# Optimization experiments

Measured on AMD Instinct MI355X. Metric: run time of the kernel, lower is better.

Reference implementation:

```python
import jax, jax.numpy as jnp
import numpy as np

N = 50000          # nodes
E = 800000         # edges (avg degree 16)
IN, HID, OUT = 128, 128, 64
LAMBDA_MAX = 2.0   # DGL default convention for scaled Laplacian (re_norm = 2/lambda_max = 1)


def setup_inputs() -> dict:
    key = jax.random.key(0)
    k1, k2, k3, k4, k5 = jax.random.split(key, 5)
    features = jax.random.normal(k1, (N, IN), dtype=jnp.float32)
    src = jax.random.randint(k2, (E,), 0, N)
    dst = jax.random.randint(k3, (E,), 0, N)
    # ChebConv(k=2) linear: Linear(2*in, out), torch default uniform init
    s1 = 1.0 / np.sqrt(2 * IN)
    W1 = jax.random.uniform(k4, (2 * IN, HID), jnp.float32, -s1, s1)
    b1 = jnp.zeros((HID,), jnp.float32)
    s2 = 1.0 / np.sqrt(2 * HID)
    W2 = jax.random.uniform(k5, (2 * HID, OUT), jnp.float32, -s2, s2)
    b2 = jnp.zeros((OUT,), jnp.float32)
    return {"features": features, "src": src, "dst": dst,
            "W1": W1, "b1": b1, "W2": W2, "b2": b2}


def _cheb_conv(x, src, dst, d_invsqrt, W, b, re_norm):
    msg = (x * d_invsqrt)[src]                                   # [E, d]
    h = jax.ops.segment_sum(msg, dst, num_segments=N) * d_invsqrt  # [N, d]
    # X_1 = L_tilde X_0 = -re_norm * A_hat X + (re_norm - 1) * X
    x1 = -re_norm * h + x * (re_norm - 1.0)
    xt = jnp.concatenate([x, x1], axis=1)                        # [N, 2d]
    return xt @ W + b


def reference(features, src, dst, W1, b1, W2, b2):
    deg = jax.ops.segment_sum(jnp.ones((E,), jnp.float32), dst, num_segments=N)
    d_invsqrt = jnp.power(jnp.clip(deg, 1.0, None), -0.5)[:, None]  # [N,1]
    re_norm = 2.0 / LAMBDA_MAX
    h = _cheb_conv(features, src, dst, d_invsqrt, W1, b1, re_norm)
    # dropout omitted (eval mode)
    h = _cheb_conv(h, src, dst, d_invsqrt, W2, b2, re_norm)
    return h
```

## Files before the change

kernel.cpp:

```cpp
#include <hip/hip_runtime.h>

#define IN_DIM  128

typedef __bf16 bf16x8 __attribute__((ext_vector_type(8)));
typedef float  f32x4  __attribute__((ext_vector_type(4)));

static inline size_t align256(size_t x) { return (x + 255) & ~size_t(255); }

__device__ __forceinline__ ushort f2b1(float f) {
    union { float f; uint u; } c; c.f = f;
    uint u = c.u;
    uint r = (u + 0x7FFFu + ((u >> 16) & 1u)) >> 16;
    return (ushort)r;
}
__device__ __forceinline__ float lo_bf(uint v) {
    union { uint u; float f; } c; c.u = v << 16; return c.f;
}
__device__ __forceinline__ float hi_bf(uint v) {
    union { uint u; float f; } c; c.u = v & 0xffff0000u; return c.f;
}


__global__ void zero_kernel(int4* __restrict__ p, int n16) {
    int i = blockIdx.x * blockDim.x + threadIdx.x;
    if (i < n16) p[i] = make_int4(0, 0, 0, 0);
}

__global__ void hist_kernel(const int* __restrict__ dst, int* __restrict__ deg,
                            int* __restrict__ rank, int E) {
    int e = blockIdx.x * blockDim.x + threadIdx.x;
    if (e < E) rank[e] = atomicAdd(&deg[dst[e]], 1);
}

__global__ __launch_bounds__(256) void scan_blocks(const int* __restrict__ deg,
                                                   int* __restrict__ pre,
                                                   int* __restrict__ bsum, int n) {
    __shared__ int sh[256];
    int t = threadIdx.x;
    int base = blockIdx.x * 1024 + t * 4;
    int v0 = 0, v1 = 0, v2 = 0, v3 = 0;
    if (base + 3 < n) {
        int4 v = *reinterpret_cast<const int4*>(deg + base);
        v0 = v.x; v1 = v.y; v2 = v.z; v3 = v.w;
    } else {
        if (base     < n) v0 = deg[base];
        if (base + 1 < n) v1 = deg[base + 1];
        if (base + 2 < n) v2 = deg[base + 2];
        if (base + 3 < n) v3 = deg[base + 3];
    }
    int s = v0 + v1 + v2 + v3;
    sh[t] = s;
    __syncthreads();
    for (int off = 1; off < 256; off <<= 1) {
        int x = (t >= off) ? sh[t - off] : 0;
        __syncthreads();
        sh[t] += x;
        __syncthreads();
    }
    int excl = sh[t] - s;
    if (t == 255) bsum[blockIdx.x] = sh[255];
    if (base     < n) pre[base]     = excl;
    if (base + 1 < n) pre[base + 1] = excl + v0;
    if (base + 2 < n) pre[base + 2] = excl + v0 + v1;
    if (base + 3 < n) pre[base + 3] = excl + v0 + v1 + v2;
}

__global__ __launch_bounds__(256) void scan_add(
    const int* __restrict__ pre, const int* __restrict__ bsum,
    const int* __restrict__ deg,
    int* __restrict__ rowptr, float* __restrict__ dinv,
    int n, int E, int nb)
{
    __shared__ int sb[64];
    int t = threadIdx.x;
    if (t < 64) {
        int orig = (t < nb) ? bsum[t] : 0;
        int v = orig;
        for (int off = 1; off < 64; off <<= 1) {
            int u = __shfl_up(v, off);
            if (t >= off) v += u;
        }
        sb[t] = v - orig;
    }
    __syncthreads();
    int i = blockIdx.x * blockDim.x + t;
    if (i < n) {
        rowptr[i] = pre[i] + sb[i >> 10];
        int d = deg[i]; if (d < 1) d = 1;
        dinv[i] = rsqrtf((float)d);
    }
    if (i == 0) rowptr[n] = E;
}


template <typename CT>
__global__ __launch_bounds__(256) void phase2_kernel(
    const int* __restrict__ src, const int* __restrict__ dst,
    const int* __restrict__ rowptr, const int* __restrict__ rank,
    CT* __restrict__ col, int E, int fillBlocks,
    const float* __restrict__ feats, const float* __restrict__ dinv,
    ushort* __restrict__ featb, ushort* __restrict__ featbs,
    ushort* __restrict__ z2s, int N, int nbF,
    const float* __restrict__ W1, ushort* __restrict__ W1t,
    const float* __restrict__ W2, ushort* __restrict__ W2ct)
{
    int b = blockIdx.x, t = threadIdx.x;
    if (b < fillBlocks) {
        int e0 = (b * 256 + t) * 4;
        if (e0 + 3 < E) {
            int4 d4 = *reinterpret_cast<const int4*>(dst + e0);
            int4 r4 = *reinterpret_cast<const int4*>(rank + e0);
            int4 s4 = *reinterpret_cast<const int4*>(src + e0);
            col[rowptr[d4.x] + r4.x] = (CT)s4.x;
            col[rowptr[d4.y] + r4.y] = (CT)s4.y;
            col[rowptr[d4.z] + r4.z] = (CT)s4.z;
            col[rowptr[d4.w] + r4.w] = (CT)s4.w;
        } else {
            for (int e = e0; e < E; ++e)
                col[rowptr[dst[e]] + rank[e]] = (CT)src[e];
        }
        return;
    }
    int b2 = b - fillBlocks;
    if (b2 < nbF) {
        size_t i4 = (size_t)b2 * 256 + t;
        if (i4 < (size_t)N * 32) {
            size_t i = i4 * 4;
            float4 v = *reinterpret_cast<const float4*>(feats + i);
            float dv = dinv[i >> 7];
            ushort4 o, os;
            o.x  = f2b1(v.x);      o.y  = f2b1(v.y);      o.z  = f2b1(v.z);      o.w  = f2b1(v.w);
            os.x = f2b1(v.x * dv); os.y = f2b1(v.y * dv); os.z = f2b1(v.z * dv); os.w = f2b1(v.w * dv);
            *reinterpret_cast<ushort4*>(featb  + i) = o;
            *reinterpret_cast<ushort4*>(featbs + i) = os;
        }
    } else if (b2 < nbF + 128) {
        if (b2 == nbF) {
            if (t < 32) *reinterpret_cast<uint2*>(featbs + (size_t)N * 128 + t * 4) = make_uint2(0, 0);
            else if (t < 48) *reinterpret_cast<uint2*>(z2s + (size_t)N * 64 + (t - 32) * 4) = make_uint2(0, 0);
        }
        int i = (b2 - nbF) * 256 + t;
        int k = i >> 7, c = i & 127;
        W1t[(size_t)c * 256 + k] = f2b1(W1[i]);
    } else {
        int i = (b2 - nbF - 128) * 256 + t;
        int c = i >> 7, k = i & 127;
        float v = (c < 64) ? W2[(size_t)k * 64 + c]
                           : W2[(size_t)(128 + k) * 64 + (c - 64)];
        W2ct[(size_t)c * 128 + k] = f2b1(v);
    }
}


__device__ __forceinline__ void sum16(
    const uint* __restrict__ Xu, int lane, int slane, int coff,
    float& a0, float& a1)
{
    uint v[16];
    #pragma unroll
    for (int j = 0; j < 16; ++j) {
        int s = __builtin_amdgcn_readlane(slane, coff + j);
        v[j] = Xu[(uint)(s * 64 + lane)];
    }
    #pragma unroll
    for (int j = 0; j < 16; ++j) {
        a0 += lo_bf(v[j]);
        a1 += hi_bf(v[j]);
    }
}

template <typename CT>
__global__ __launch_bounds__(256) void agg_sum128(
    const ushort* __restrict__ Xs, const int* __restrict__ rowptr,
    const CT* __restrict__ col, const float* __restrict__ dinv,
    ushort* __restrict__ X1, int nNodes)
{
    int wid  = (blockIdx.x * blockDim.x + threadIdx.x) >> 6;
    int lane = threadIdx.x & 63;
    if (wid >= nNodes) return;
    wid = __builtin_amdgcn_readfirstlane(wid);
    int e0 = rowptr[wid], e1 = rowptr[wid + 1];
    float sc = -dinv[wid];
    const uint* Xu = reinterpret_cast<const uint*>(Xs);

    float a0 = 0.f, a1 = 0.f;
    for (int base = e0; base < e1; base += 64) {
        int idx = base + lane;
        int s = (idx < e1) ? (int)col[(idx < e1) ? idx : e0] : nNodes;
        int cnt = e1 - base; if (cnt > 64) cnt = 64;
        sum16(Xu, lane, s, 0, a0, a1);
        if (cnt > 16) sum16(Xu, lane, s, 16, a0, a1);
        if (cnt > 32) sum16(Xu, lane, s, 32, a0, a1);
        if (cnt > 48) sum16(Xu, lane, s, 48, a0, a1);
    }
    uint o = (uint)f2b1(a0 * sc) | ((uint)f2b1(a1 * sc) << 16);
    reinterpret_cast<uint*>(X1)[(uint)(wid * 64 + lane)] = o;
}


__device__ __forceinline__ void sum16z(
    const ushort* __restrict__ Z, int lane, int slane, int coff, float& a0)
{
    ushort v[16];
    #pragma unroll
    for (int j = 0; j < 16; ++j) {
        int s = __builtin_amdgcn_readlane(slane, coff + j);
        v[j] = Z[(uint)(s * 64 + lane)];
    }
    #pragma unroll
    for (int j = 0; j < 16; ++j)
        a0 += lo_bf((uint)v[j]);
}

template <typename CT>
__global__ __launch_bounds__(256) void agg_sum64(
    const ushort* __restrict__ Z2, const int* __restrict__ rowptr,
    const CT* __restrict__ col, const float* __restrict__ dinv,
    float* __restrict__ Y, int nNodes)
{
    int wid  = (blockIdx.x * blockDim.x + threadIdx.x) >> 6;
    int lane = threadIdx.x & 63;
    if (wid >= nNodes) return;
    wid = __builtin_amdgcn_readfirstlane(wid);
    int e0 = rowptr[wid], e1 = rowptr[wid + 1];
    float sc = -dinv[wid];

    float a0 = 0.f;
    for (int base = e0; base < e1; base += 64) {
        int idx = base + lane;
        int s = (idx < e1) ? (int)col[(idx < e1) ? idx : e0] : nNodes;
        int cnt = e1 - base; if (cnt > 64) cnt = 64;
        sum16z(Z2, lane, s, 0, a0);
        if (cnt > 16) sum16z(Z2, lane, s, 16, a0);
        if (cnt > 32) sum16z(Z2, lane, s, 32, a0);
        if (cnt > 48) sum16z(Z2, lane, s, 48, a0);
    }
    Y[(uint)(wid * 64 + lane)] += a0 * sc;
}


__global__ __launch_bounds__(256) void gemm_mfma1(
    const ushort* __restrict__ XA, const ushort* __restrict__ XB,
    const ushort* __restrict__ Wt, const float* __restrict__ bias,
    ushort* __restrict__ Y, int nNodes)
{
    __shared__ ushort wlds[128 * 256];
    int t = threadIdx.x;

    #pragma unroll
    for (int it = 0; it < 16; ++it) {
        int i = it * 256 + t;
        int c = i >> 5;
        int o = (i & 31) << 4;
        bf16x8 v = *reinterpret_cast<const bf16x8*>(Wt + ((size_t)c << 8) + (o >> 1));
        *reinterpret_cast<bf16x8*>((char*)wlds + ((size_t)c << 9) + (o ^ ((c & 7) << 4))) = v;
    }
    __syncthreads();

    int wave = t >> 6, lane = t & 63;
    int r16 = lane & 15, g = lane >> 4;
    int nodeBase = blockIdx.x * 128 + wave * 32;

    int arow0 = nodeBase + r16;       if (arow0 > nNodes - 1) arow0 = nNodes - 1;
    int arow1 = nodeBase + 16 + r16;  if (arow1 > nNodes - 1) arow1 = nNodes - 1;
    const ushort* pA0 = XA + (size_t)arow0 * 128;
    const ushort* pA1 = XA + (size_t)arow1 * 128;
    const ushort* pB0 = XB + (size_t)arow0 * 128;
    const ushort* pB1 = XB + (size_t)arow1 * 128;

    f32x4 acc0[8], acc1[8];
    #pragma unroll
    for (int i = 0; i < 8; ++i) { acc0[i] = f32x4{0,0,0,0}; acc1[i] = f32x4{0,0,0,0}; }

    #pragma unroll
    for (int kb = 0; kb < 8; ++kb) {
        int kk = (kb & 3) * 32 + g * 8;
        bf16x8 a0 = *reinterpret_cast<const bf16x8*>(((kb < 4) ? pA0 : pB0) + kk);
        bf16x8 a1 = *reinterpret_cast<const bf16x8*>(((kb < 4) ? pA1 : pB1) + kk);
        int o = kb * 64 + g * 16;
        #pragma unroll
        for (int ct = 0; ct < 8; ++ct) {
            int c = ct * 16 + r16;
            bf16x8 b = *reinterpret_cast<const bf16x8*>(
                (const char*)wlds + ((size_t)c << 9) + (o ^ ((c & 7) << 4)));
            acc0[ct] = __builtin_amdgcn_mfma_f32_16x16x32_bf16(a0, b, acc0[ct], 0, 0, 0);
            acc1[ct] = __builtin_amdgcn_mfma_f32_16x16x32_bf16(a1, b, acc1[ct], 0, 0, 0);
        }
    }

    #pragma unroll
    for (int ct = 0; ct < 8; ++ct) {
        float bv = bias[ct * 16 + r16];
        #pragma unroll
        for (int r = 0; r < 4; ++r) {
            int orow0 = nodeBase + g * 4 + r;
            int orow1 = orow0 + 16;
            if (orow0 < nNodes) Y[(size_t)orow0 * 128 + ct * 16 + r16] = f2b1(acc0[ct][r] + bv);
            if (orow1 < nNodes) Y[(size_t)orow1 * 128 + ct * 16 + r16] = f2b1(acc1[ct][r] + bv);
        }
    }
}


__global__ __launch_bounds__(256) void gemm_mfma2(
    const ushort* __restrict__ H1, const ushort* __restrict__ W2ct,
    const float* __restrict__ bias, const float* __restrict__ dinv,
    float* __restrict__ Yout, ushort* __restrict__ Z2, int nNodes)
{
    __shared__ ushort wlds[128 * 128];
    int t = threadIdx.x;

    #pragma unroll
    for (int it = 0; it < 8; ++it) {
        int i = it * 256 + t;
        int c = i >> 4;
        int o = (i & 15) << 4;
        bf16x8 v = *reinterpret_cast<const bf16x8*>(W2ct + ((size_t)c << 7) + (o >> 1));
        *reinterpret_cast<bf16x8*>((char*)wlds + ((size_t)c << 8) + (o ^ ((c & 7) << 4))) = v;
    }
    __syncthreads();

    int wave = t >> 6, lane = t & 63;
    int r16 = lane & 15, g = lane >> 4;
    int nodeBase = blockIdx.x * 128 + wave * 32;

    int arow0 = nodeBase + r16;       if (arow0 > nNodes - 1) arow0 = nNodes - 1;
    int arow1 = nodeBase + 16 + r16;  if (arow1 > nNodes - 1) arow1 = nNodes - 1;
    const ushort* p0 = H1 + (size_t)arow0 * 128;
    const ushort* p1 = H1 + (size_t)arow1 * 128;

    f32x4 acc0[8], acc1[8];
    #pragma unroll
    for (int i = 0; i < 8; ++i) { acc0[i] = f32x4{0,0,0,0}; acc1[i] = f32x4{0,0,0,0}; }

    #pragma unroll
    for (int kb = 0; kb < 4; ++kb) {
        int kk = kb * 32 + g * 8;
        bf16x8 a0 = *reinterpret_cast<const bf16x8*>(p0 + kk);
        bf16x8 a1 = *reinterpret_cast<const bf16x8*>(p1 + kk);
        int o = kb * 64 + g * 16;
        #pragma unroll
        for (int ct = 0; ct < 8; ++ct) {
            int c = ct * 16 + r16;
            bf16x8 b = *reinterpret_cast<const bf16x8*>(
                (const char*)wlds + ((size_t)c << 8) + (o ^ ((c & 7) << 4)));
            acc0[ct] = __builtin_amdgcn_mfma_f32_16x16x32_bf16(a0, b, acc0[ct], 0, 0, 0);
            acc1[ct] = __builtin_amdgcn_mfma_f32_16x16x32_bf16(a1, b, acc1[ct], 0, 0, 0);
        }
    }

    float dv0[4], dv1[4];
    #pragma unroll
    for (int r = 0; r < 4; ++r) {
        int o0 = nodeBase + g * 4 + r;      if (o0 > nNodes - 1) o0 = nNodes - 1;
        int o1 = nodeBase + 16 + g * 4 + r; if (o1 > nNodes - 1) o1 = nNodes - 1;
        dv0[r] = dinv[o0]; dv1[r] = dinv[o1];
    }

    #pragma unroll
    for (int ct = 0; ct < 8; ++ct) {
        float bv = (ct < 4) ? bias[ct * 16 + r16] : 0.f;
        #pragma unroll
        for (int r = 0; r < 4; ++r) {
            int orow0 = nodeBase + g * 4 + r;
            int orow1 = orow0 + 16;
            if (ct < 4) {
                if (orow0 < nNodes) Yout[(size_t)orow0 * 64 + ct * 16 + r16] = acc0[ct][r] + bv;
                if (orow1 < nNodes) Yout[(size_t)orow1 * 64 + ct * 16 + r16] = acc1[ct][r] + bv;
            } else {
                if (orow0 < nNodes) Z2[(size_t)orow0 * 64 + (ct - 4) * 16 + r16] = f2b1(acc0[ct][r] * dv0[r]);
                if (orow1 < nNodes) Z2[(size_t)orow1 * 64 + (ct - 4) * 16 + r16] = f2b1(acc1[ct][r] * dv1[r]);
            }
        }
    }
}


extern "C" void kernel_launch(void* const* d_in, const int* in_sizes, int n_in,
                              void* d_out, int out_size, void* d_ws, size_t ws_size,
                              hipStream_t stream)
{
    const float* feats = (const float*)d_in[0];
    const int*   src   = (const int*)d_in[1];
    const int*   dst   = (const int*)d_in[2];
    const float* W1    = (const float*)d_in[3];
    const float* b1    = (const float*)d_in[4];
    const float* W2    = (const float*)d_in[5];
    const float* b2    = (const float*)d_in[6];
    float* out = (float*)d_out;

    const int N = in_sizes[0] / IN_DIM;
    const int E = in_sizes[1];
    const int NB = (N + 1023) / 1024;

    char* ws = (char*)d_ws;
    size_t off = 0;
    int*    deg    = (int*)(ws + off);    off = align256(off + (size_t)N * 4);
    int*    rowptr = (int*)(ws + off);    off = align256(off + (size_t)(N + 1) * 4);
    int*    pre    = (int*)(ws + off);    off = align256(off + (size_t)N * 4);
    int*    bsum   = (int*)(ws + off);    off = align256(off + (size_t)64 * 4);
    int*    rank   = (int*)(ws + off);    off = align256(off + (size_t)E * 4);
    void*   colv   = (void*)(ws + off);   off = align256(off + (size_t)E * 4);
    float*  dinv   = (float*)(ws + off);  off = align256(off + (size_t)N * 4);
    ushort* featb  = (ushort*)(ws + off); off = align256(off + (size_t)N * 128 * 2);
    ushort* featbs = (ushort*)(ws + off); off = align256(off + (size_t)(N + 1) * 128 * 2);
    ushort* x1b    = (ushort*)(ws + off); off = align256(off + (size_t)N * 128 * 2);
    ushort* h1b    = (ushort*)(ws + off); off = align256(off + (size_t)N * 128 * 2);
    ushort* z2s    = (ushort*)(ws + off); off = align256(off + (size_t)(N + 1) * 64 * 2);
    ushort* W1t    = (ushort*)(ws + off); off = align256(off + (size_t)256 * 128 * 2);
    ushort* W2ct   = (ushort*)(ws + off); off = align256(off + (size_t)128 * 128 * 2);

    const int n16 = (N + 3) / 4;
    zero_kernel<<<(n16 + 255) / 256, 256, 0, stream>>>((int4*)deg, n16);
    hist_kernel<<<(E + 255) / 256, 256, 0, stream>>>(dst, deg, rank, E);
    scan_blocks<<<NB, 256, 0, stream>>>(deg, pre, bsum, N);
    scan_add<<<(N + 255) / 256, 256, 0, stream>>>(pre, bsum, deg, rowptr, dinv, N, E, NB);

    const bool small = (N <= 65535);
    const int fillBlocks = ((E + 3) / 4 + 255) / 256;
    const int nbF = (N * 32 + 255) / 256;
    const int p2Blocks = fillBlocks + nbF + 128 + 64;
    if (small)
        phase2_kernel<ushort><<<p2Blocks, 256, 0, stream>>>(
            src, dst, rowptr, rank, (ushort*)colv, E, fillBlocks,
            feats, dinv, featb, featbs, z2s, N, nbF, W1, W1t, W2, W2ct);
    else
        phase2_kernel<uint><<<p2Blocks, 256, 0, stream>>>(
            src, dst, rowptr, rank, (uint*)colv, E, fillBlocks,
            feats, dinv, featb, featbs, z2s, N, nbF, W1, W1t, W2, W2ct);

    const int aggBlocks = (N * 64 + 255) / 256;
    const int gemmBlocks = (N + 127) / 128;

    if (small)
        agg_sum128<ushort><<<aggBlocks, 256, 0, stream>>>(featbs, rowptr, (const ushort*)colv, dinv, x1b, N);
    else
        agg_sum128<uint><<<aggBlocks, 256, 0, stream>>>(featbs, rowptr, (const uint*)colv, dinv, x1b, N);
    gemm_mfma1<<<gemmBlocks, 256, 0, stream>>>(featb, x1b, W1t, b1, h1b, N);

    gemm_mfma2<<<gemmBlocks, 256, 0, stream>>>(h1b, W2ct, b2, dinv, out, z2s, N);
    if (small)
        agg_sum64<ushort><<<aggBlocks, 256, 0, stream>>>(z2s, rowptr, (const ushort*)colv, dinv, out, N);
    else
        agg_sum64<uint><<<aggBlocks, 256, 0, stream>>>(z2s, rowptr, (const uint*)colv, dinv, out, N);
}
```

Baseline: 145.9 us.

## Split gathered feature tables into 64-byte column blocks for cache-local aggregation

```diff
diff --git a/kernel.cpp b/kernel.cpp
--- a/kernel.cpp
+++ b/kernel.cpp
@@ -99,8 +99,8 @@
     const int* __restrict__ rowptr, const int* __restrict__ rank,
     CT* __restrict__ col, int E, int fillBlocks,
     const float* __restrict__ feats, const float* __restrict__ dinv,
-    ushort* __restrict__ featb, ushort* __restrict__ featbs,
-    ushort* __restrict__ z2s, int N, int nbF,
+    ushort* __restrict__ featb, ushort* __restrict__ featbs2,
+    ushort* __restrict__ z2s2, int N, int nbF,
     const float* __restrict__ W1, ushort* __restrict__ W1t,
     const float* __restrict__ W2, ushort* __restrict__ W2ct)
 {
@@ -127,17 +127,26 @@
         if (i4 < (size_t)N * 32) {
             size_t i = i4 * 4;
             float4 v = *reinterpret_cast<const float4*>(feats + i);
-            float dv = dinv[i >> 7];
+            int node = (int)(i4 >> 5);
+            int j = (int)(i4 & 31);
+            float dv = dinv[node];
             ushort4 o, os;
             o.x  = f2b1(v.x);      o.y  = f2b1(v.y);      o.z  = f2b1(v.z);      o.w  = f2b1(v.w);
             os.x = f2b1(v.x * dv); os.y = f2b1(v.y * dv); os.z = f2b1(v.z * dv); os.w = f2b1(v.w * dv);
-            *reinterpret_cast<ushort4*>(featb  + i) = o;
-            *reinterpret_cast<ushort4*>(featbs + i) = os;
+            *reinterpret_cast<ushort4*>(featb + i) = o;
+            int blk = j >> 3, jj = j & 7;
+            *reinterpret_cast<ushort4*>(featbs2 + ((size_t)(blk * (N + 1) + node)) * 32 + jj * 4) = os;
         }
     } else if (b2 < nbF + 128) {
-        if (b2 == nbF) {
-            if (t < 32) *reinterpret_cast<uint2*>(featbs + (size_t)N * 128 + t * 4) = make_uint2(0, 0);
-            else if (t < 48) *reinterpret_cast<uint2*>(z2s + (size_t)N * 64 + (t - 32) * 4) = make_uint2(0, 0);
+        if (b2 == nbF && t < 48) {
+            if (t < 32) {
+                int blk = t >> 3, j = t & 7;
+                *reinterpret_cast<uint2*>(featbs2 + ((size_t)(blk * (N + 1) + N)) * 32 + j * 4) = make_uint2(0, 0);
+            } else {
+                int tt = t - 32;
+                int blk = tt >> 3, j = tt & 7;
+                *reinterpret_cast<uint2*>(z2s2 + ((size_t)(blk * (N + 1) + N)) * 32 + j * 4) = make_uint2(0, 0);
+            }
         }
         int i = (b2 - nbF) * 256 + t;
         int k = i >> 7, c = i & 127;
@@ -152,25 +161,25 @@
 }
 
 
-__device__ __forceinline__ void sum16(
-    const uint* __restrict__ Xu, int lane, int slane, int coff,
+__device__ __forceinline__ void grp4(
+    const uint* __restrict__ base, int sl, int g, int d, int eslot,
     float& a0, float& a1)
 {
-    uint v[16];
-    #pragma unroll
-    for (int j = 0; j < 16; ++j) {
-        int s = __builtin_amdgcn_readlane(slane, coff + j);
-        v[j] = Xu[(uint)(s * 64 + lane)];
-    }
-    #pragma unroll
-    for (int j = 0; j < 16; ++j) {
-        a0 += lo_bf(v[j]);
-        a1 += hi_bf(v[j]);
+    uint v[4];
+    #pragma unroll
+    for (int c = 0; c < 4; ++c) {
+        int s = __shfl(sl, g * 16 + c * 4 + eslot);
+        v[c] = base[(uint)(s * 16 + d)];
+    }
+    #pragma unroll
+    for (int c = 0; c < 4; ++c) {
+        a0 += lo_bf(v[c]);
+        a1 += hi_bf(v[c]);
     }
 }
 
 template <typename CT>
-__global__ __launch_bounds__(256) void agg_sum128(
+__global__ __launch_bounds__(256) void agg1_blk(
     const ushort* __restrict__ Xs, const int* __restrict__ rowptr,
     const CT* __restrict__ col, const float* __restrict__ dinv,
     ushort* __restrict__ X1, int nNodes)
@@ -178,64 +187,69 @@
     int wid  = (blockIdx.x * blockDim.x + threadIdx.x) >> 6;
     int lane = threadIdx.x & 63;
     if (wid >= nNodes) return;
-    wid = __builtin_amdgcn_readfirstlane(wid);
-    int e0 = rowptr[wid], e1 = rowptr[wid + 1];
-    float sc = -dinv[wid];
-    const uint* Xu = reinterpret_cast<const uint*>(Xs);
+    int n = __builtin_amdgcn_readfirstlane(wid);
+    int b = blockIdx.y;
+    int e0 = rowptr[n], e1 = rowptr[n + 1];
+    float sc = -dinv[n];
+    const uint* base = reinterpret_cast<const uint*>(Xs) + (size_t)b * (nNodes + 1) * 16;
+    int d = lane & 15, eslot = lane >> 4;
 
     float a0 = 0.f, a1 = 0.f;
-    for (int base = e0; base < e1; base += 64) {
-        int idx = base + lane;
-        int s = (idx < e1) ? (int)col[(idx < e1) ? idx : e0] : nNodes;
-        int cnt = e1 - base; if (cnt > 64) cnt = 64;
-        sum16(Xu, lane, s, 0, a0, a1);
-        if (cnt > 16) sum16(Xu, lane, s, 16, a0, a1);
-        if (cnt > 32) sum16(Xu, lane, s, 32, a0, a1);
-        if (cnt > 48) sum16(Xu, lane, s, 48, a0, a1);
-    }
-    uint o = (uint)f2b1(a0 * sc) | ((uint)f2b1(a1 * sc) << 16);
-    reinterpret_cast<uint*>(X1)[(uint)(wid * 64 + lane)] = o;
-}
-
-
-__device__ __forceinline__ void sum16z(
-    const ushort* __restrict__ Z, int lane, int slane, int coff, float& a0)
-{
-    ushort v[16];
-    #pragma unroll
-    for (int j = 0; j < 16; ++j) {
-        int s = __builtin_amdgcn_readlane(slane, coff + j);
-        v[j] = Z[(uint)(s * 64 + lane)];
-    }
-    #pragma unroll
-    for (int j = 0; j < 16; ++j)
-        a0 += lo_bf((uint)v[j]);
+    for (int bs = e0; bs < e1; bs += 64) {
+        int idx = bs + lane;
+        int ci = (idx < e1) ? idx : e0;
+        int cv = (int)col[ci];
+        int sl = (idx < e1) ? cv : nNodes;
+        int cnt = e1 - bs; if (cnt > 64) cnt = 64;
+        grp4(base, sl, 0, d, eslot, a0, a1);
+        if (cnt > 16) grp4(base, sl, 1, d, eslot, a0, a1);
+        if (cnt > 32) grp4(base, sl, 2, d, eslot, a0, a1);
+        if (cnt > 48) grp4(base, sl, 3, d, eslot, a0, a1);
+    }
+    a0 += __shfl_xor(a0, 16); a0 += __shfl_xor(a0, 32);
+    a1 += __shfl_xor(a1, 16); a1 += __shfl_xor(a1, 32);
+    if (eslot == 0) {
+        uint o = (uint)f2b1(a0 * sc) | ((uint)f2b1(a1 * sc) << 16);
+        reinterpret_cast<uint*>(X1)[(uint)(n * 64 + b * 16 + d)] = o;
+    }
 }
 
 template <typename CT>
-__global__ __launch_bounds__(256) void agg_sum64(
-    const ushort* __restrict__ Z2, const int* __restrict__ rowptr,
+__global__ __launch_bounds__(256) void agg2_blk(
+    const ushort* __restrict__ Zs, const int* __restrict__ rowptr,
     const CT* __restrict__ col, const float* __restrict__ dinv,
     float* __restrict__ Y, int nNodes)
 {
     int wid  = (blockIdx.x * blockDim.x + threadIdx.x) >> 6;
     int lane = threadIdx.x & 63;
     if (wid >= nNodes) return;
-    wid = __builtin_amdgcn_readfirstlane(wid);
-    int e0 = rowptr[wid], e1 = rowptr[wid + 1];
-    float sc = -dinv[wid];
-
-    float a0 = 0.f;
-    for (int base = e0; base < e1; base += 64) {
-        int idx = base + lane;
-        int s = (idx < e1) ? (int)col[(idx < e1) ? idx : e0] : nNodes;
-        int cnt = e1 - base; if (cnt > 64) cnt = 64;
-        sum16z(Z2, lane, s, 0, a0);
-        if (cnt > 16) sum16z(Z2, lane, s, 16, a0);
-        if (cnt > 32) sum16z(Z2, lane, s, 32, a0);
-        if (cnt > 48) sum16z(Z2, lane, s, 48, a0);
-    }
-    Y[(uint)(wid * 64 + lane)] += a0 * sc;
+    int n = __builtin_amdgcn_readfirstlane(wid);
+    int b = blockIdx.y;
+    int e0 = rowptr[n], e1 = rowptr[n + 1];
+    float sc = -dinv[n];
+    const uint* base = reinterpret_cast<const uint*>(Zs) + (size_t)b * (nNodes + 1) * 16;
+    int d = lane & 15, eslot = lane >> 4;
+
+    float a0 = 0.f, a1 = 0.f;
+    for (int bs = e0; bs < e1; bs += 64) {
+        int idx = bs + lane;
+        int ci = (idx < e1) ? idx : e0;
+        int cv = (int)col[ci];
+        int sl = (idx < e1) ? cv : nNodes;
+        int cnt = e1 - bs; if (cnt > 64) cnt = 64;
+        grp4(base, sl, 0, d, eslot, a0, a1);
+        if (cnt > 16) grp4(base, sl, 1, d, eslot, a0, a1);
+        if (cnt > 32) grp4(base, sl, 2, d, eslot, a0, a1);
+        if (cnt > 48) grp4(base, sl, 3, d, eslot, a0, a1);
+    }
+    a0 += __shfl_xor(a0, 16); a0 += __shfl_xor(a0, 32);
+    a1 += __shfl_xor(a1, 16); a1 += __shfl_xor(a1, 32);
+    if (eslot == 0) {
+        float2* p = reinterpret_cast<float2*>(Y) + (uint)(n * 32 + b * 16 + d);
+        float2 y = *p;
+        y.x += a0 * sc; y.y += a1 * sc;
+        *p = y;
+    }
 }
 
 
@@ -368,8 +382,12 @@
                 if (orow0 < nNodes) Yout[(size_t)orow0 * 64 + ct * 16 + r16] = acc0[ct][r] + bv;
                 if (orow1 < nNodes) Yout[(size_t)orow1 * 64 + ct * 16 + r16] = acc1[ct][r] + bv;
             } else {
-                if (orow0 < nNodes) Z2[(size_t)orow0 * 64 + (ct - 4) * 16 + r16] = f2b1(acc0[ct][r] * dv0[r]);
-                if (orow1 < nNodes) Z2[(size_t)orow1 * 64 + (ct - 4) * 16 + r16] = f2b1(acc1[ct][r] * dv1[r]);
+                int blk = (ct - 4) >> 1;
+                int c32 = ((ct - 4) & 1) * 16 + r16;
+                if (orow0 < nNodes)
+                    Z2[((size_t)(blk * (nNodes + 1) + orow0)) * 32 + c32] = f2b1(acc0[ct][r] * dv0[r]);
+                if (orow1 < nNodes)
+                    Z2[((size_t)(blk * (nNodes + 1) + orow1)) * 32 + c32] = f2b1(acc1[ct][r] * dv1[r]);
             }
         }
     }
@@ -403,10 +421,10 @@
     void*   colv   = (void*)(ws + off);   off = align256(off + (size_t)E * 4);
     float*  dinv   = (float*)(ws + off);  off = align256(off + (size_t)N * 4);
     ushort* featb  = (ushort*)(ws + off); off = align256(off + (size_t)N * 128 * 2);
-    ushort* featbs = (ushort*)(ws + off); off = align256(off + (size_t)(N + 1) * 128 * 2);
+    ushort* featbs2= (ushort*)(ws + off); off = align256(off + (size_t)4 * (N + 1) * 32 * 2);
     ushort* x1b    = (ushort*)(ws + off); off = align256(off + (size_t)N * 128 * 2);
     ushort* h1b    = (ushort*)(ws + off); off = align256(off + (size_t)N * 128 * 2);
-    ushort* z2s    = (ushort*)(ws + off); off = align256(off + (size_t)(N + 1) * 64 * 2);
+    ushort* z2s2   = (ushort*)(ws + off); off = align256(off + (size_t)2 * (N + 1) * 32 * 2);
     ushort* W1t    = (ushort*)(ws + off); off = align256(off + (size_t)256 * 128 * 2);
     ushort* W2ct   = (ushort*)(ws + off); off = align256(off + (size_t)128 * 128 * 2);
 
@@ -423,24 +441,24 @@
     if (small)
         phase2_kernel<ushort><<<p2Blocks, 256, 0, stream>>>(
             src, dst, rowptr, rank, (ushort*)colv, E, fillBlocks,
-            feats, dinv, featb, featbs, z2s, N, nbF, W1, W1t, W2, W2ct);
+            feats, dinv, featb, featbs2, z2s2, N, nbF, W1, W1t, W2, W2ct);
     else
         phase2_kernel<uint><<<p2Blocks, 256, 0, stream>>>(
             src, dst, rowptr, rank, (uint*)colv, E, fillBlocks,
-            feats, dinv, featb, featbs, z2s, N, nbF, W1, W1t, W2, W2ct);
-
-    const int aggBlocks = (N * 64 + 255) / 256;
+            feats, dinv, featb, featbs2, z2s2, N, nbF, W1, W1t, W2, W2ct);
+
+    const int aggXBlocks = (N * 64 + 255) / 256;
     const int gemmBlocks = (N + 127) / 128;
 
     if (small)
-        agg_sum128<ushort><<<aggBlocks, 256, 0, stream>>>(featbs, rowptr, (const ushort*)colv, dinv, x1b, N);
+        agg1_blk<ushort><<<dim3(aggXBlocks, 4), 256, 0, stream>>>(featbs2, rowptr, (const ushort*)colv, dinv, x1b, N);
     else
-        agg_sum128<uint><<<aggBlocks, 256, 0, stream>>>(featbs, rowptr, (const uint*)colv, dinv, x1b, N);
+        agg1_blk<uint><<<dim3(aggXBlocks, 4), 256, 0, stream>>>(featbs2, rowptr, (const uint*)colv, dinv, x1b, N);
     gemm_mfma1<<<gemmBlocks, 256, 0, stream>>>(featb, x1b, W1t, b1, h1b, N);
 
-    gemm_mfma2<<<gemmBlocks, 256, 0, stream>>>(h1b, W2ct, b2, dinv, out, z2s, N);
+    gemm_mfma2<<<gemmBlocks, 256, 0, stream>>>(h1b, W2ct, b2, dinv, out, z2s2, N);
     if (small)
-        agg_sum64<ushort><<<aggBlocks, 256, 0, stream>>>(z2s, rowptr, (const ushort*)colv, dinv, out, N);
+        agg2_blk<ushort><<<dim3(aggXBlocks, 2), 256, 0, stream>>>(z2s2, rowptr, (const ushort*)colv, dinv, out, N);
     else
-        agg_sum64<uint><<<aggBlocks, 256, 0, stream>>>(z2s, rowptr, (const uint*)colv, dinv, out, N);
-}
+        agg2_blk<uint><<<dim3(aggXBlocks, 2), 256, 0, stream>>>(z2s2, rowptr, (const uint*)colv, dinv, out, N);
+}
```

Measured after the change: 180.7 us. 1.24x slower.

## Vectorize neighbor gathers with 16-byte loads and cross-lane edge-group reduction

Applied to the files above, without the earlier changes.

```diff
diff --git a/kernel.cpp b/kernel.cpp
--- a/kernel.cpp
+++ b/kernel.cpp
@@ -152,23 +152,6 @@
 }
 
 
-__device__ __forceinline__ void sum16(
-    const uint* __restrict__ Xu, int lane, int slane, int coff,
-    float& a0, float& a1)
-{
-    uint v[16];
-    #pragma unroll
-    for (int j = 0; j < 16; ++j) {
-        int s = __builtin_amdgcn_readlane(slane, coff + j);
-        v[j] = Xu[(uint)(s * 64 + lane)];
-    }
-    #pragma unroll
-    for (int j = 0; j < 16; ++j) {
-        a0 += lo_bf(v[j]);
-        a1 += hi_bf(v[j]);
-    }
-}
-
 template <typename CT>
 __global__ __launch_bounds__(256) void agg_sum128(
     const ushort* __restrict__ Xs, const int* __restrict__ rowptr,
@@ -178,64 +161,96 @@
     int wid  = (blockIdx.x * blockDim.x + threadIdx.x) >> 6;
     int lane = threadIdx.x & 63;
     if (wid >= nNodes) return;
-    wid = __builtin_amdgcn_readfirstlane(wid);
-    int e0 = rowptr[wid], e1 = rowptr[wid + 1];
-    float sc = -dinv[wid];
-    const uint* Xu = reinterpret_cast<const uint*>(Xs);
-
-    float a0 = 0.f, a1 = 0.f;
+    int n = __builtin_amdgcn_readfirstlane(wid);
+    int e0 = rowptr[n], e1 = rowptr[n + 1];
+    float sc = -dinv[n];
+    const uint4* X4 = reinterpret_cast<const uint4*>(Xs);
+    int d = lane & 15, g = lane >> 4;
+
+    float a[8];
+    #pragma unroll
+    for (int i = 0; i < 8; ++i) a[i] = 0.f;
+
     for (int base = e0; base < e1; base += 64) {
         int idx = base + lane;
-        int s = (idx < e1) ? (int)col[(idx < e1) ? idx : e0] : nNodes;
+        int cvl = (int)col[(idx < e1) ? idx : e0];
+        int cv = (idx < e1) ? cvl : nNodes;
         int cnt = e1 - base; if (cnt > 64) cnt = 64;
-        sum16(Xu, lane, s, 0, a0, a1);
-        if (cnt > 16) sum16(Xu, lane, s, 16, a0, a1);
-        if (cnt > 32) sum16(Xu, lane, s, 32, a0, a1);
-        if (cnt > 48) sum16(Xu, lane, s, 48, a0, a1);
-    }
-    uint o = (uint)f2b1(a0 * sc) | ((uint)f2b1(a1 * sc) << 16);
-    reinterpret_cast<uint*>(X1)[(uint)(wid * 64 + lane)] = o;
-}
-
-
-__device__ __forceinline__ void sum16z(
-    const ushort* __restrict__ Z, int lane, int slane, int coff, float& a0)
-{
-    ushort v[16];
-    #pragma unroll
-    for (int j = 0; j < 16; ++j) {
-        int s = __builtin_amdgcn_readlane(slane, coff + j);
-        v[j] = Z[(uint)(s * 64 + lane)];
-    }
-    #pragma unroll
-    for (int j = 0; j < 16; ++j)
-        a0 += lo_bf((uint)v[j]);
-}
+        int jmax = (cnt + 3) >> 2;
+        #pragma unroll 4
+        for (int j = 0; j < jmax; ++j) {
+            int s = __shfl(cv, j * 4 + g);
+            uint4 v = X4[(uint)(s * 16 + d)];
+            a[0] += lo_bf(v.x); a[1] += hi_bf(v.x);
+            a[2] += lo_bf(v.y); a[3] += hi_bf(v.y);
+            a[4] += lo_bf(v.z); a[5] += hi_bf(v.z);
+            a[6] += lo_bf(v.w); a[7] += hi_bf(v.w);
+        }
+    }
+    #pragma unroll
+    for (int i = 0; i < 8; ++i) {
+        a[i] += __shfl_xor(a[i], 16);
+        a[i] += __shfl_xor(a[i], 32);
+    }
+    if (g == 0) {
+        uint4 o;
+        o.x = (uint)f2b1(a[0] * sc) | ((uint)f2b1(a[1] * sc) << 16);
+        o.y = (uint)f2b1(a[2] * sc) | ((uint)f2b1(a[3] * sc) << 16);
+        o.z = (uint)f2b1(a[4] * sc) | ((uint)f2b1(a[5] * sc) << 16);
+        o.w = (uint)f2b1(a[6] * sc) | ((uint)f2b1(a[7] * sc) << 16);
+        reinterpret_cast<uint4*>(X1)[(uint)(n * 16 + d)] = o;
+    }
+}
+
 
 template <typename CT>
 __global__ __launch_bounds__(256) void agg_sum64(
-    const ushort* __restrict__ Z2, const int* __restrict__ rowptr,
+    const ushort* __restrict__ Zs, const int* __restrict__ rowptr,
     const CT* __restrict__ col, const float* __restrict__ dinv,
     float* __restrict__ Y, int nNodes)
 {
     int wid  = (blockIdx.x * blockDim.x + threadIdx.x) >> 6;
     int lane = threadIdx.x & 63;
     if (wid >= nNodes) return;
-    wid = __builtin_amdgcn_readfirstlane(wid);
-    int e0 = rowptr[wid], e1 = rowptr[wid + 1];
-    float sc = -dinv[wid];
-
-    float a0 = 0.f;
+    int n = __builtin_amdgcn_readfirstlane(wid);
+    int e0 = rowptr[n], e1 = rowptr[n + 1];
+    float sc = -dinv[n];
+    const uint4* Z4 = reinterpret_cast<const uint4*>(Zs);
+    int d = lane & 7, g = lane >> 3;
+
+    float a[8];
+    #pragma unroll
+    for (int i = 0; i < 8; ++i) a[i] = 0.f;
+
     for (int base = e0; base < e1; base += 64) {
         int idx = base + lane;
-        int s = (idx < e1) ? (int)col[(idx < e1) ? idx : e0] : nNodes;
+        int cvl = (int)col[(idx < e1) ? idx : e0];
+        int cv = (idx < e1) ? cvl : nNodes;
         int cnt = e1 - base; if (cnt > 64) cnt = 64;
-        sum16z(Z2, lane, s, 0, a0);
-        if (cnt > 16) sum16z(Z2, lane, s, 16, a0);
-        if (cnt > 32) sum16z(Z2, lane, s, 32, a0);
-        if (cnt > 48) sum16z(Z2, lane, s, 48, a0);
-    }
-    Y[(uint)(wid * 64 + lane)] += a0 * sc;
+        int jmax = (cnt + 7) >> 3;
+        #pragma unroll 4
+        for (int j = 0; j < jmax; ++j) {
+            int s = __shfl(cv, j * 8 + g);
+            uint4 v = Z4[(uint)(s * 8 + d)];
+            a[0] += lo_bf(v.x); a[1] += hi_bf(v.x);
+            a[2] += lo_bf(v.y); a[3] += hi_bf(v.y);
+            a[4] += lo_bf(v.z); a[5] += hi_bf(v.z);
+            a[6] += lo_bf(v.w); a[7] += hi_bf(v.w);
+        }
+    }
+    #pragma unroll
+    for (int i = 0; i < 8; ++i) {
+        a[i] += __shfl_xor(a[i], 8);
+        a[i] += __shfl_xor(a[i], 16);
+        a[i] += __shfl_xor(a[i], 32);
+    }
+    if (g == 0) {
+        float4* Y4 = reinterpret_cast<float4*>(Y) + (uint)(n * 16 + d * 2);
+        float4 y0 = Y4[0], y1 = Y4[1];
+        y0.x += a[0] * sc; y0.y += a[1] * sc; y0.z += a[2] * sc; y0.w += a[3] * sc;
+        y1.x += a[4] * sc; y1.y += a[5] * sc; y1.z += a[6] * sc; y1.w += a[7] * sc;
+        Y4[0] = y0; Y4[1] = y1;
+    }
 }
 
 
```

Result: slower. 151.5 us (+3.8%).

## Process two destination nodes per wavefront in both aggregation kernels

Applied to the files above, without the earlier changes.

```diff
diff --git a/kernel.cpp b/kernel.cpp
--- a/kernel.cpp
+++ b/kernel.cpp
@@ -152,90 +152,139 @@
 }
 
 
-__device__ __forceinline__ void sum16(
-    const uint* __restrict__ Xu, int lane, int slane, int coff,
-    float& a0, float& a1)
-{
-    uint v[16];
-    #pragma unroll
-    for (int j = 0; j < 16; ++j) {
-        int s = __builtin_amdgcn_readlane(slane, coff + j);
-        v[j] = Xu[(uint)(s * 64 + lane)];
-    }
-    #pragma unroll
-    for (int j = 0; j < 16; ++j) {
-        a0 += lo_bf(v[j]);
-        a1 += hi_bf(v[j]);
-    }
-}
-
 template <typename CT>
 __global__ __launch_bounds__(256) void agg_sum128(
     const ushort* __restrict__ Xs, const int* __restrict__ rowptr,
     const CT* __restrict__ col, const float* __restrict__ dinv,
     ushort* __restrict__ X1, int nNodes)
 {
-    int wid  = (blockIdx.x * blockDim.x + threadIdx.x) >> 6;
+    int w    = (blockIdx.x * blockDim.x + threadIdx.x) >> 6;
     int lane = threadIdx.x & 63;
-    if (wid >= nNodes) return;
-    wid = __builtin_amdgcn_readfirstlane(wid);
-    int e0 = rowptr[wid], e1 = rowptr[wid + 1];
-    float sc = -dinv[wid];
+    int n0 = w * 2;
+    if (n0 >= nNodes) return;
+    n0 = __builtin_amdgcn_readfirstlane(n0);
+    bool has1 = (n0 + 1) < nNodes;
+    int e0a = rowptr[n0];
+    int e1a = rowptr[n0 + 1];
+    int e1b = has1 ? rowptr[n0 + 2] : e1a;
+    float sca = -dinv[n0];
+    float scb = -dinv[has1 ? n0 + 1 : n0];
     const uint* Xu = reinterpret_cast<const uint*>(Xs);
 
-    float a0 = 0.f, a1 = 0.f;
-    for (int base = e0; base < e1; base += 64) {
-        int idx = base + lane;
-        int s = (idx < e1) ? (int)col[(idx < e1) ? idx : e0] : nNodes;
-        int cnt = e1 - base; if (cnt > 64) cnt = 64;
-        sum16(Xu, lane, s, 0, a0, a1);
-        if (cnt > 16) sum16(Xu, lane, s, 16, a0, a1);
-        if (cnt > 32) sum16(Xu, lane, s, 32, a0, a1);
-        if (cnt > 48) sum16(Xu, lane, s, 48, a0, a1);
-    }
-    uint o = (uint)f2b1(a0 * sc) | ((uint)f2b1(a1 * sc) << 16);
-    reinterpret_cast<uint*>(X1)[(uint)(wid * 64 + lane)] = o;
-}
-
-
-__device__ __forceinline__ void sum16z(
-    const ushort* __restrict__ Z, int lane, int slane, int coff, float& a0)
-{
-    ushort v[16];
-    #pragma unroll
-    for (int j = 0; j < 16; ++j) {
-        int s = __builtin_amdgcn_readlane(slane, coff + j);
-        v[j] = Z[(uint)(s * 64 + lane)];
-    }
-    #pragma unroll
-    for (int j = 0; j < 16; ++j)
-        a0 += lo_bf((uint)v[j]);
-}
+    float a0 = 0.f, a1 = 0.f, b0 = 0.f, b1 = 0.f;
+    int basea = e0a, baseb = e1a;
+    while (basea < e1a || baseb < e1b) {
+        int half = lane >> 5, sl = lane & 31;
+        int idx = half ? (baseb + sl) : (basea + sl);
+        int ee  = half ? e1b : e1a;
+        bool okl = idx < ee;
+        int cvl = (int)col[okl ? idx : 0];
+        int cv  = okl ? cvl : nNodes;
+        int cnta = e1a - basea, cntb = e1b - baseb;
+        {
+            uint va[16], vb[16];
+            #pragma unroll
+            for (int j = 0; j < 16; ++j) {
+                int s0 = __builtin_amdgcn_readlane(cv, j);
+                int s1 = __builtin_amdgcn_readlane(cv, 32 + j);
+                va[j] = Xu[(uint)(s0 * 64 + lane)];
+                vb[j] = Xu[(uint)(s1 * 64 + lane)];
+            }
+            #pragma unroll
+            for (int j = 0; j < 16; ++j) {
+                a0 += lo_bf(va[j]); a1 += hi_bf(va[j]);
+                b0 += lo_bf(vb[j]); b1 += hi_bf(vb[j]);
+            }
+        }
+        if (cnta > 16 || cntb > 16) {
+            uint va[16], vb[16];
+            #pragma unroll
+            for (int j = 0; j < 16; ++j) {
+                int s0 = __builtin_amdgcn_readlane(cv, 16 + j);
+                int s1 = __builtin_amdgcn_readlane(cv, 48 + j);
+                va[j] = Xu[(uint)(s0 * 64 + lane)];
+                vb[j] = Xu[(uint)(s1 * 64 + lane)];
+            }
+            #pragma unroll
+            for (int j = 0; j < 16; ++j) {
+                a0 += lo_bf(va[j]); a1 += hi_bf(va[j]);
+                b0 += lo_bf(vb[j]); b1 += hi_bf(vb[j]);
+            }
+        }
+        basea += 32; baseb += 32;
+    }
+    uint oA = (uint)f2b1(a0 * sca) | ((uint)f2b1(a1 * sca) << 16);
+    reinterpret_cast<uint*>(X1)[(uint)(n0 * 64 + lane)] = oA;
+    if (has1) {
+        uint oB = (uint)f2b1(b0 * scb) | ((uint)f2b1(b1 * scb) << 16);
+        reinterpret_cast<uint*>(X1)[(uint)((n0 + 1) * 64 + lane)] = oB;
+    }
+}
+
 
 template <typename CT>
 __global__ __launch_bounds__(256) void agg_sum64(
-    const ushort* __restrict__ Z2, const int* __restrict__ rowptr,
+    const ushort* __restrict__ Zs, const int* __restrict__ rowptr,
     const CT* __restrict__ col, const float* __restrict__ dinv,
     float* __restrict__ Y, int nNodes)
 {
-    int wid  = (blockIdx.x * blockDim.x + threadIdx.x) >> 6;
+    int w    = (blockIdx.x * blockDim.x + threadIdx.x) >> 6;
     int lane = threadIdx.x & 63;
-    if (wid >= nNodes) return;
-    wid = __builtin_amdgcn_readfirstlane(wid);
-    int e0 = rowptr[wid], e1 = rowptr[wid + 1];
-    float sc = -dinv[wid];
-
-    float a0 = 0.f;
-    for (int base = e0; base < e1; base += 64) {
-        int idx = base + lane;
-        int s = (idx < e1) ? (int)col[(idx < e1) ? idx : e0] : nNodes;
-        int cnt = e1 - base; if (cnt > 64) cnt = 64;
-        sum16z(Z2, lane, s, 0, a0);
-        if (cnt > 16) sum16z(Z2, lane, s, 16, a0);
-        if (cnt > 32) sum16z(Z2, lane, s, 32, a0);
-        if (cnt > 48) sum16z(Z2, lane, s, 48, a0);
-    }
-    Y[(uint)(wid * 64 + lane)] += a0 * sc;
+    int n0 = w * 2;
+    if (n0 >= nNodes) return;
+    n0 = __builtin_amdgcn_readfirstlane(n0);
+    bool has1 = (n0 + 1) < nNodes;
+    int e0a = rowptr[n0];
+    int e1a = rowptr[n0 + 1];
+    int e1b = has1 ? rowptr[n0 + 2] : e1a;
+    float sca = -dinv[n0];
+    float scb = -dinv[has1 ? n0 + 1 : n0];
+
+    float fa = 0.f, fb = 0.f;
+    int basea = e0a, baseb = e1a;
+    while (basea < e1a || baseb < e1b) {
+        int half = lane >> 5, sl = lane & 31;
+        int idx = half ? (baseb + sl) : (basea + sl);
+        int ee  = half ? e1b : e1a;
+        bool okl = idx < ee;
+        int cvl = (int)col[okl ? idx : 0];
+        int cv  = okl ? cvl : nNodes;
+        int cnta = e1a - basea, cntb = e1b - baseb;
+        {
+            ushort va[16], vb[16];
+            #pragma unroll
+            for (int j = 0; j < 16; ++j) {
+                int s0 = __builtin_amdgcn_readlane(cv, j);
+                int s1 = __builtin_amdgcn_readlane(cv, 32 + j);
+                va[j] = Zs[(uint)(s0 * 64 + lane)];
+                vb[j] = Zs[(uint)(s1 * 64 + lane)];
+            }
+            #pragma unroll
+            for (int j = 0; j < 16; ++j) {
+                fa += lo_bf((uint)va[j]);
+                fb += lo_bf((uint)vb[j]);
+            }
+        }
+        if (cnta > 16 || cntb > 16) {
+            ushort va[16], vb[16];
+            #pragma unroll
+            for (int j = 0; j < 16; ++j) {
+                int s0 = __builtin_amdgcn_readlane(cv, 16 + j);
+                int s1 = __builtin_amdgcn_readlane(cv, 48 + j);
+                va[j] = Zs[(uint)(s0 * 64 + lane)];
+                vb[j] = Zs[(uint)(s1 * 64 + lane)];
+            }
+            #pragma unroll
+            for (int j = 0; j < 16; ++j) {
+                fa += lo_bf((uint)va[j]);
+                fb += lo_bf((uint)vb[j]);
+            }
+        }
+        basea += 32; baseb += 32;
+    }
+    Y[(uint)(n0 * 64 + lane)] += fa * sca;
+    if (has1)
+        Y[(uint)((n0 + 1) * 64 + lane)] += fb * scb;
 }
 
 
@@ -429,7 +478,8 @@
             src, dst, rowptr, rank, (uint*)colv, E, fillBlocks,
             feats, dinv, featb, featbs, z2s, N, nbF, W1, W1t, W2, W2ct);
 
-    const int aggBlocks = (N * 64 + 255) / 256;
+    const int nPairWaves = (N + 1) / 2;
+    const int aggBlocks = (nPairWaves * 64 + 255) / 256;
     const int gemmBlocks = (N + 127) / 128;
 
     if (small)
```

New measurement: 142.9 us. -2.0%, faster.
